# Kernel tuning notes

Hardware: AMD Instinct MI355X
Metric: run time of the kernel (lower is better)

Reference implementation:

```python
import jax, jax.numpy as jnp
import numpy as np

B, M, L, D, H, DFF, K, NL = 32, 512, 512, 128, 8, 256, 16, 2


def setup_inputs() -> dict:
    key = jax.random.key(0)
    ks = jax.random.split(key, 12)
    s = 0.02
    p = lambda i, shape: (jax.random.normal(ks[i], shape, jnp.float32) * s)
    return {
        "enc_out_vari": jax.random.normal(ks[0], (B, M, D), jnp.float32),
        "x_enc": jax.random.normal(ks[1], (B, L, M), jnp.float32),
        "conv1_W": p(2, (D, D)), "conv1_b": jnp.zeros((D,), jnp.float32),
        "conv2_W": p(3, (D, D)), "conv2_b": jnp.zeros((D,), jnp.float32),
        "Wq": p(4, (NL, D, D)), "Wk": p(5, (NL, D, D)),
        "Wv": p(6, (NL, D, D)), "Wo": p(7, (NL, D, D)),
        "ffn_W1": p(8, (NL, D, DFF)), "ffn_b1": jnp.zeros((NL, DFF), jnp.float32),
        "ffn_W2": p(9, (NL, DFF, D)), "ffn_b2": jnp.zeros((NL, D), jnp.float32),
        "ln1_g": jnp.ones((NL, D), jnp.float32), "ln1_b": jnp.zeros((NL, D), jnp.float32),
        "ln2_g": jnp.ones((NL, D), jnp.float32), "ln2_b": jnp.zeros((NL, D), jnp.float32),
    }


def _ln(x, g, b, eps=1e-5):
    mu = x.mean(-1, keepdims=True)
    var = ((x - mu) ** 2).mean(-1, keepdims=True)
    return (x - mu) * jax.lax.rsqrt(var + eps) * g + b


def _gcn_conv(x, src, dst, W, b, N):
    # PyG GCNConv: XW, add self loops, symmetric D^-1/2 (A+I) D^-1/2 aggregation, + bias
    h = x @ W
    loop = jnp.arange(N)
    s = jnp.concatenate([src, loop])
    d = jnp.concatenate([dst, loop])
    deg = jax.ops.segment_sum(jnp.ones_like(d, jnp.float32), d, num_segments=N)
    dinv = jnp.where(deg > 0, jax.lax.rsqrt(deg), 0.0)
    norm = dinv[s] * dinv[d]
    out = jax.ops.segment_sum(h[s] * norm[:, None], d, num_segments=N)
    return out + b


def _forward(enc_out_vari, x_enc, conv1_W, conv1_b, conv2_W, conv2_b,
             Wq, Wk, Wv, Wo, ffn_W1, ffn_b1, ffn_W2, ffn_b2,
             ln1_g, ln1_b, ln2_g, ln2_b):
    # --- dynamic graph from Pearson correlation (faithful: ascending argsort, idx 1..k) ---
    x = x_enc.transpose(0, 2, 1)                      # [B, M, L]
    c = x - x.mean(-1, keepdims=True)
    cov = jnp.einsum('bml,bnl->bmn', c, c) / (L - 1)  # [B, M, M]
    std = jnp.sqrt(jnp.diagonal(cov, axis1=-2, axis2=-1))
    std = jnp.where(std == 0, 1.0, std)
    corr = cov / (std[:, :, None] * std[:, None, :])
    neighbors = jnp.argsort(corr, axis=-1)[:, :, 1:K + 1]  # [B, M, K]
    row = jnp.tile(jnp.arange(M), K)                  # arange(M).repeat(k) in torch
    col = neighbors.reshape(B, M * K)
    offs = (jnp.arange(B) * M)[:, None]               # batch the graphs into one
    src = (row[None, :] + offs).reshape(-1)
    dst = (col + offs).reshape(-1)
    N = B * M
    # --- 2-layer GCN over flattened node set ---
    x_raw = enc_out_vari.reshape(N, D)
    h1 = jax.nn.relu(_gcn_conv(x_raw, src, dst, conv1_W, conv1_b, N))
    h2 = jax.nn.relu(_gcn_conv(h1, src, dst, conv2_W, conv2_b, N))
    xg = h2.reshape(B, M, D)
    # --- cross-attention transformer encoder: query stream = enc_out_vari, kv = GCN output ---
    h = enc_out_vari
    hd = D // H
    scale = 1.0 / jnp.sqrt(jnp.float32(hd))
    for l in range(NL):
        q = (h @ Wq[l]).reshape(B, M, H, hd)
        k_ = (xg @ Wk[l]).reshape(B, M, H, hd)
        v = (xg @ Wv[l]).reshape(B, M, H, hd)
        att = jax.nn.softmax(jnp.einsum('bqhd,bkhd->bhqk', q, k_) * scale, axis=-1)
        o = jnp.einsum('bhqk,bkhd->bqhd', att, v).reshape(B, M, D) @ Wo[l]
        h = _ln(h + o, ln1_g[l], ln1_b[l])
        f = jax.nn.relu(h @ ffn_W1[l] + ffn_b1[l]) @ ffn_W2[l] + ffn_b2[l]
        h = _ln(h + f, ln2_g[l], ln2_b[l])
    return h


def reference(enc_out_vari, x_enc, conv1_W, conv1_b, conv2_W, conv2_b,
              Wq, Wk, Wv, Wo, ffn_W1, ffn_b1, ffn_W2, ffn_b2,
              ln1_g, ln1_b, ln2_g, ln2_b):
    return _forward(enc_out_vari, x_enc, conv1_W, conv1_b, conv2_W, conv2_b,
                    Wq, Wk, Wv, Wo, ffn_W1, ffn_b1, ffn_W2, ffn_b2,
                    ln1_g, ln1_b, ln2_g, ln2_b)
```

## Files before the change

### kernel.cpp

```cpp
#include <hip/hip_runtime.h>
#include <float.h>

#define BB 32
#define MMv 512
#define LLv 512
#define DDv 128
#define HHv 8
#define DFFv 256
#define KNB 16
#define NLAY 2
#define NNODE (BB*MMv)
#define TOTE  (NNODE*KNB)
#define WTOT  294912

typedef unsigned short ushort_t;
typedef unsigned int u32;
typedef __attribute__((ext_vector_type(8))) short bf16x8;
typedef __attribute__((ext_vector_type(4))) float f32x4;

__device__ __forceinline__ float bf2f(ushort_t u){
  union { u32 i; float f; } x; x.i = ((u32)u) << 16; return x.f;
}
__device__ __forceinline__ ushort_t f2bf(float f){
  union { u32 i; float f; } x; x.f = f;
  u32 r = x.i + 0x7FFFu + ((x.i >> 16) & 1u);
  return (ushort_t)(r >> 16);
}
__device__ __forceinline__ float ldx(const void* p, size_t i, int f32){
  return f32 ? ((const float*)p)[i] : bf2f(((const ushort_t*)p)[i]);
}
__device__ __forceinline__ float wsum(float v){
  #pragma unroll
  for(int s=32;s;s>>=1) v += __shfl_xor(v,s);
  return v;
}

__global__ __launch_bounds__(256) void diag_fill_k(float* out, int n, float val){
  for(int i = blockIdx.x*256 + threadIdx.x; i < n; i += gridDim.x*256) out[i] = val;
}

struct P18 { const ushort_t* p[18]; int n[18]; };
__global__ __launch_bounds__(256) void ddet_k(P18 a, int* DF){
  int i = blockIdx.x;
  const ushort_t* q = a.p[i];
  int P = min(a.n[i], 4096);
  int t = threadIdx.x;
  int r1 = 0, evenNZ = 0, oddNZ = 0;
  for(int j=t; j<P; j+=256){
    ushort_t v = q[j];
    if(((v >> 7) & 0xFF) >= 0xC0) r1 = 1;
    if(v){ if(j & 1) oddNZ = 1; else evenNZ = 1; }
  }
  __shared__ int sh[3];
  if(t==0){ sh[0]=0; sh[1]=0; sh[2]=0; }
  __syncthreads();
  if(r1) atomicOr(&sh[0],1);
  if(evenNZ) atomicOr(&sh[1],1);
  if(oddNZ) atomicOr(&sh[2],1);
  __syncthreads();
  if(t==0) DF[i] = sh[0] | ((sh[1]==0) & (sh[2]!=0));
}

__global__ __launch_bounds__(256) void prep_k(const void* c1W, const void* c2W,
    const void* Wq, const void* Wk, const void* Wv, const void* Wo,
    const void* W1, const void* W2, ushort_t* Wth, ushort_t* Wtl, const int* DF){
  __shared__ ushort_t th[32][33];
  __shared__ ushort_t tl[32][33];
  int job = blockIdx.z;
  const void* src; int dfi; size_t soff, doff; int K, N;
  switch(job){
    case 0:  src=c1W; dfi=2;  soff=0; K=128; N=128; doff=0; break;
    case 1:  src=c2W; dfi=4;  soff=0; K=128; N=128; doff=16384; break;
    case 2: case 3:
      src=Wq; dfi=6; soff=(size_t)(job-2)*16384; K=128; N=128;
      doff=32768 + (size_t)(job-2)*49152; break;
    case 4: case 5:
      src=Wk; dfi=7; soff=(size_t)(job-4)*16384; K=128; N=128;
      doff=32768 + (size_t)(job-4)*49152 + 16384; break;
    case 6: case 7:
      src=Wv; dfi=8; soff=(size_t)(job-6)*16384; K=128; N=128;
      doff=32768 + (size_t)(job-6)*49152 + 32768; break;
    case 8: case 9:
      src=Wo; dfi=9; soff=(size_t)(job-8)*16384; K=128; N=128;
      doff=131072 + (size_t)(job-8)*16384; break;
    case 10: case 11:
      src=W1; dfi=10; soff=(size_t)(job-10)*32768; K=128; N=256;
      doff=163840 + (size_t)(job-10)*32768; break;
    default:
      src=W2; dfi=12; soff=(size_t)(job-12)*32768; K=256; N=128;
      doff=229376 + (size_t)(job-12)*32768; break;
  }
  int n0 = blockIdx.x*32, k0 = blockIdx.y*32;
  if(n0 >= N || k0 >= K) return;
  int f32 = DF[dfi];
  int tx = threadIdx.x, ty = threadIdx.y;
  #pragma unroll
  for(int i=0;i<4;i++){
    int k = k0+ty+8*i, n = n0+tx;
    float x = ldx(src, soff + (size_t)k*N + n, f32);
    ushort_t hi = f2bf(x);
    ushort_t lo = f2bf(x - bf2f(hi));
    th[ty+8*i][tx] = hi; tl[ty+8*i][tx] = lo;
  }
  __syncthreads();
  #pragma unroll
  for(int i=0;i<4;i++){
    int n = n0+ty+8*i, k = k0+tx;
    size_t d = doff + (size_t)n*K + k;
    Wth[d] = th[tx][ty+8*i];
    Wtl[d] = tl[tx][ty+8*i];
  }
}

__global__ __launch_bounds__(256) void split_k(const void* xe, ushort_t* Xhi,
                                               ushort_t* Xlo, const int* DF){
  __shared__ ushort_t th[32][33];
  __shared__ ushort_t tl[32][33];
  int f32 = DF[1];
  int b = blockIdx.z;
  int m0 = blockIdx.x*32, l0 = blockIdx.y*32;
  int tx = threadIdx.x, ty = threadIdx.y;
  #pragma unroll
  for(int i=0;i<4;i++){
    int l = l0+ty+8*i, m = m0+tx;
    float x = ldx(xe, (size_t)b*LLv*MMv + (size_t)l*MMv + m, f32);
    ushort_t hi = f2bf(x);
    ushort_t lo = f2bf(x - bf2f(hi));
    th[ty+8*i][tx] = hi; tl[ty+8*i][tx] = lo;
  }
  __syncthreads();
  #pragma unroll
  for(int i=0;i<4;i++){
    size_t d = (size_t)b*MMv*LLv + (size_t)(m0+ty+8*i)*LLv + l0+tx;
    Xhi[d] = th[tx][ty+8*i];
    Xlo[d] = tl[tx][ty+8*i];
  }
}

__global__ __launch_bounds__(256) void stats2_k(const ushort_t* Xhi, const ushort_t* Xlo,
                                                double* S64, double* R64){
  int row = blockIdx.x*4 + (threadIdx.x >> 6);
  int lane = threadIdx.x & 63;
  const ushort_t* Hr = Xhi + (size_t)row*LLv + lane*8;
  const ushort_t* Lr = Xlo + (size_t)row*LLv + lane*8;
  float s = 0.f, ss = 0.f;
  #pragma unroll
  for(int j=0;j<8;j++){
    float x = bf2f(Hr[j]) + bf2f(Lr[j]);
    s += x; ss = fmaf(x, x, ss);
  }
  s = wsum(s); ss = wsum(ss);
  if(lane == 0){
    S64[row] = (double)s;
    float cov = (ss - s*s*(1.0f/LLv)) * (1.0f/(LLv-1));
    float sd = (cov > 0.f) ? sqrtf(cov) : 0.f;
    R64[row] = (sd > 0.f) ? (double)(1.0f/sd) : 1.0;
  }
}

__global__ __launch_bounds__(1024, 8) void corrsel_k(const ushort_t* Xhi, const ushort_t* Xlo,
                                                     const double* S64, const double* R64,
                                                     int* nbr, const int* DF){
  __shared__ __attribute__((aligned(16))) char smem[66560];
  ushort_t* Ah = (ushort_t*)smem;
  ushort_t* Al = Ah + 32*520;
  float*    Cs = (float*)smem;
  int f32 = DF[1];
  int lin = blockIdx.y*16 + blockIdx.x;
  int xcd = lin & 7, slot = lin >> 3;
  int b = xcd + 8*(slot >> 4);
  int strip = slot & 15;
  int m0 = strip*32;
  int t = threadIdx.x;
  int wave = t >> 6, lane = t & 63;
  int quad = lane >> 4, l16 = lane & 15;
  const ushort_t* Hb = Xhi + (size_t)b*MMv*LLv;
  const ushort_t* Lb = Xlo + (size_t)b*MMv*LLv;
  for(int idx=t; idx<2048; idx+=1024){
    int mm = idx >> 6, c8 = (idx & 63)*8;
    *(bf16x8*)&Ah[mm*520 + c8] = *(const bf16x8*)&Hb[(size_t)(m0+mm)*LLv + c8];
    *(bf16x8*)&Al[mm*520 + c8] = *(const bf16x8*)&Lb[(size_t)(m0+mm)*LLv + c8];
  }
  __syncthreads();
  const double* Sb = S64 + b*MMv;
  const double* Rb = R64 + b*MMv;
  int nbase = wave*32;
  float corr[16];
  int nnv[2];
  #pragma unroll
  for(int cs=0; cs<2; cs++){
    int nn = nbase + cs*16 + l16;
    nnv[cs] = nn;
    size_t brow = (size_t)nn*LLv + quad*8;
    f32x4 acc0 = {0.f,0.f,0.f,0.f};
    f32x4 acc1 = {0.f,0.f,0.f,0.f};
    if(f32){
      #pragma unroll
      for(int kk=0; kk<16; kk++){
        int ko = kk*32 + quad*8;
        bf16x8 bh = *(const bf16x8*)&Hb[brow + kk*32];
        bf16x8 bl = *(const bf16x8*)&Lb[brow + kk*32];
        bf16x8 ah0 = *(const bf16x8*)&Ah[l16*520 + ko];
        bf16x8 al0 = *(const bf16x8*)&Al[l16*520 + ko];
        bf16x8 ah1 = *(const bf16x8*)&Ah[(16+l16)*520 + ko];
        bf16x8 al1 = *(const bf16x8*)&Al[(16+l16)*520 + ko];
        acc0 = __builtin_amdgcn_mfma_f32_16x16x32_bf16(ah0, bh, acc0, 0, 0, 0);
        acc0 = __builtin_amdgcn_mfma_f32_16x16x32_bf16(ah0, bl, acc0, 0, 0, 0);
        acc0 = __builtin_amdgcn_mfma_f32_16x16x32_bf16(al0, bh, acc0, 0, 0, 0);
        acc1 = __builtin_amdgcn_mfma_f32_16x16x32_bf16(ah1, bh, acc1, 0, 0, 0);
        acc1 = __builtin_amdgcn_mfma_f32_16x16x32_bf16(ah1, bl, acc1, 0, 0, 0);
        acc1 = __builtin_amdgcn_mfma_f32_16x16x32_bf16(al1, bh, acc1, 0, 0, 0);
      }
    } else {
      #pragma unroll
      for(int g=0; g<4; g++){
        bf16x8 bh[4];
        #pragma unroll
        for(int j=0;j<4;j++) bh[j] = *(const bf16x8*)&Hb[brow + g*128 + j*32];
        #pragma unroll
        for(int j=0;j<4;j++){
          int ko = g*128 + j*32 + quad*8;
          bf16x8 ah0 = *(const bf16x8*)&Ah[l16*520 + ko];
          bf16x8 ah1 = *(const bf16x8*)&Ah[(16+l16)*520 + ko];
          acc0 = __builtin_amdgcn_mfma_f32_16x16x32_bf16(ah0, bh[j], acc0, 0, 0, 0);
          acc1 = __builtin_amdgcn_mfma_f32_16x16x32_bf16(ah1, bh[j], acc1, 0, 0, 0);
        }
      }
    }
    float sn = (float)(Sb[nn]*(1.0/LLv));
    float rn = (float)Rb[nn];
    #pragma unroll
    for(int r=0;r<4;r++){
      int ml0 = quad*4 + r;
      float cov0 = (acc0[r] - (float)Sb[m0+ml0]*sn) * (1.0f/(LLv-1));
      corr[cs*8 + r] = cov0 * (float)Rb[m0+ml0] * rn;
      int ml1 = 16 + ml0;
      float cov1 = (acc1[r] - (float)Sb[m0+ml1]*sn) * (1.0f/(LLv-1));
      corr[cs*8 + 4 + r] = cov1 * (float)Rb[m0+ml1] * rn;
    }
  }
  __syncthreads();
  #pragma unroll
  for(int cs=0; cs<2; cs++){
    #pragma unroll
    for(int r=0;r<4;r++){
      int ml0 = quad*4 + r;
      Cs[ml0*516 + nnv[cs]] = corr[cs*8 + r];
      Cs[(16+ml0)*516 + nnv[cs]] = corr[cs*8 + 4 + r];
    }
  }
  __syncthreads();
  for(int rr=0; rr<2; rr++){
    int r = wave*2 + rr;
    float vals[8];
    #pragma unroll
    for(int j=0;j<8;j++) vals[j] = Cs[r*516 + lane + 64*j];
    for(int it=0; it<=KNB; it++){
      float bvv = FLT_MAX; int bi = 0x7fffffff;
      #pragma unroll
      for(int j=0;j<8;j++){
        int n = lane + 64*j;
        if(vals[j] < bvv){ bvv = vals[j]; bi = n; }
      }
      #pragma unroll
      for(int s=32; s; s>>=1){
        float v2 = __shfl_xor(bvv, s);
        int   i2 = __shfl_xor(bi,  s);
        if(v2 < bvv || (v2 == bvv && i2 < bi)){ bvv = v2; bi = i2; }
      }
      int gbi = bi;
      int bic = min(max(gbi, 0), MMv-1);
      if(it > 0 && lane == 0) nbr[(size_t)(b*MMv + m0 + r)*KNB + it-1] = bic;
      if((gbi & 63) == lane && gbi < MMv){
        int jj = gbi >> 6;
        #pragma unroll
        for(int j=0;j<8;j++) if(j == jj) vals[j] = FLT_MAX;
      }
    }
  }
}

__global__ __launch_bounds__(256) void zero_k(int* p){
  p[blockIdx.x*256 + threadIdx.x] = 0;
}

__global__ __launch_bounds__(256) void hist_k(const int* nbr, int* cnt){
  int tid = blockIdx.x*256 + threadIdx.x;
  int b = tid >> 13;
  int col = min(max(nbr[tid], 0), MMv-1);
  atomicAdd(&cnt[b*MMv + col], 1);
}

__global__ __launch_bounds__(256) void scan_k(const int* cnt, int* off,
                                              int* cursor, float* dinv){
  __shared__ int part[256];
  int t = threadIdx.x;
  int base = t*64, s = 0;
  for(int i=0;i<64;i++) s += cnt[base+i];
  part[t] = s; __syncthreads();
  for(int st=1; st<256; st<<=1){
    int v = (t >= st) ? part[t-st] : 0;
    __syncthreads();
    part[t] += v; __syncthreads();
  }
  int run = (t > 0) ? part[t-1] : 0;
  for(int i=0;i<64;i++){
    int idx = base+i;
    off[idx] = run; cursor[idx] = run;
    run += cnt[idx];
    dinv[idx] = 1.0f/sqrtf((float)(cnt[idx]+1));
  }
  if(t == 255) off[NNODE] = run;
}

__global__ __launch_bounds__(256) void fill_k(const int* nbr, int* cursor, int* esrc){
  int tid = blockIdx.x*256 + threadIdx.x;
  int b = tid >> 13;
  int rem = tid & 8191;
  int col = min(max(nbr[tid], 0), MMv-1);
  int dst = b*MMv + col;
  int srcl = rem & 511;
  int pos = atomicAdd(&cursor[dst], 1);
  pos = min(max(pos, 0), TOTE-1);
  esrc[pos] = b*MMv + srcl;
}

__global__ __launch_bounds__(256) void gemm_k(const float* A,
                                              const ushort_t* Wth, const ushort_t* Wtl,
                                              size_t woffT, int wdi,
                                              const void* bias, int boff, int bdi,
                                              float* C, int Kd, int Dout, int relu,
                                              const int* DF){
  __shared__ __attribute__((aligned(16))) ushort_t Ah[64*72];
  __shared__ __attribute__((aligned(16))) ushort_t Al[64*72];
  __shared__ __attribute__((aligned(16))) ushort_t Wh[32*72];
  __shared__ __attribute__((aligned(16))) ushort_t Wl[32*72];
  int wf32 = DF[wdi];
  int bf32 = DF[bdi];
  int m0 = blockIdx.y*64, n0 = blockIdx.x*32;
  int t = threadIdx.x;
  int wave = t >> 6, lane = t & 63;
  int quad = lane >> 4, l16 = lane & 15;
  f32x4 acc[2];
  #pragma unroll
  for(int nt=0;nt<2;nt++) acc[nt] = (f32x4){0.f,0.f,0.f,0.f};
  for(int kc=0; kc<Kd; kc+=64){
    for(int s=t; s<1024; s+=256){
      int row = s >> 4, c4 = (s & 15)*4;
      float4 av = *(const float4*)&A[(size_t)(m0+row)*Kd + kc + c4];
      ushort_t h0=f2bf(av.x), h1=f2bf(av.y), h2=f2bf(av.z), h3=f2bf(av.w);
      ushort_t g0=f2bf(av.x-bf2f(h0)), g1=f2bf(av.y-bf2f(h1));
      ushort_t g2=f2bf(av.z-bf2f(h2)), g3=f2bf(av.w-bf2f(h3));
      *(ushort4*)&Ah[row*72 + c4] = make_ushort4(h0,h1,h2,h3);
      *(ushort4*)&Al[row*72 + c4] = make_ushort4(g0,g1,g2,g3);
    }
    for(int s=t; s<256; s+=256){
      int row = s >> 3, c8 = (s & 7)*8;
      size_t g = woffT + (size_t)(n0+row)*Kd + kc + c8;
      *(bf16x8*)&Wh[row*72 + c8] = *(const bf16x8*)&Wth[g];
      if(wf32) *(bf16x8*)&Wl[row*72 + c8] = *(const bf16x8*)&Wtl[g];
    }
    __syncthreads();
    #pragma unroll
    for(int kk=0; kk<64; kk+=32){
      int ko = kk + quad*8;
      bf16x8 ah = *(const bf16x8*)&Ah[(wave*16+l16)*72 + ko];
      bf16x8 al = *(const bf16x8*)&Al[(wave*16+l16)*72 + ko];
      #pragma unroll
      for(int nt=0; nt<2; nt++){
        bf16x8 wh = *(const bf16x8*)&Wh[(nt*16+l16)*72 + ko];
        acc[nt] = __builtin_amdgcn_mfma_f32_16x16x32_bf16(ah, wh, acc[nt], 0, 0, 0);
        acc[nt] = __builtin_amdgcn_mfma_f32_16x16x32_bf16(al, wh, acc[nt], 0, 0, 0);
        if(wf32){
          bf16x8 wl = *(const bf16x8*)&Wl[(nt*16+l16)*72 + ko];
          acc[nt] = __builtin_amdgcn_mfma_f32_16x16x32_bf16(ah, wl, acc[nt], 0, 0, 0);
        }
      }
    }
    __syncthreads();
  }
  #pragma unroll
  for(int nt=0; nt<2; nt++){
    int n = n0 + nt*16 + l16;
    float bv = bias ? ldx(bias, boff + n, bf32) : 0.f;
    #pragma unroll
    for(int r=0; r<2*2; r++){
      float v = acc[nt][r] + bv;
      if(relu) v = fmaxf(v, 0.f);
      C[(size_t)(m0 + wave*16 + quad*4 + r)*Dout + n] = v;
    }
  }
}

__global__ __launch_bounds__(256) void qkv_k(const float* hF, const float* xg,
                                             const ushort_t* Wth, const ushort_t* Wtl,
                                             size_t qoff, float* t0, float* kv,
                                             const int* DF){
  __shared__ __attribute__((aligned(16))) ushort_t Ah[64*72];
  __shared__ __attribute__((aligned(16))) ushort_t Al[64*72];
  __shared__ __attribute__((aligned(16))) ushort_t Wh[32*72];
  __shared__ __attribute__((aligned(16))) ushort_t Wl[32*72];
  int m0 = blockIdx.y*64, n0 = blockIdx.x*32;
  int wdi = (n0 < 128) ? 6 : ((n0 < 256) ? 7 : 8);
  int wf32 = DF[wdi];
  const float* A = (n0 < 128) ? hF : xg;
  int t = threadIdx.x;
  int wave = t >> 6, lane = t & 63;
  int quad = lane >> 4, l16 = lane & 15;
  f32x4 acc[2];
  #pragma unroll
  for(int nt=0;nt<2;nt++) acc[nt] = (f32x4){0.f,0.f,0.f,0.f};
  for(int kc=0; kc<DDv; kc+=64){
    for(int s=t; s<1024; s+=256){
      int row = s >> 4, c4 = (s & 15)*4;
      float4 av = *(const float4*)&A[(size_t)(m0+row)*DDv + kc + c4];
      ushort_t h0=f2bf(av.x), h1=f2bf(av.y), h2=f2bf(av.z), h3=f2bf(av.w);
      ushort_t g0=f2bf(av.x-bf2f(h0)), g1=f2bf(av.y-bf2f(h1));
      ushort_t g2=f2bf(av.z-bf2f(h2)), g3=f2bf(av.w-bf2f(h3));
      *(ushort4*)&Ah[row*72 + c4] = make_ushort4(h0,h1,h2,h3);
      *(ushort4*)&Al[row*72 + c4] = make_ushort4(g0,g1,g2,g3);
    }
    for(int s=t; s<256; s+=256){
      int row = s >> 3, c8 = (s & 7)*8;
      size_t g = qoff + (size_t)(n0+row)*DDv + kc + c8;
      *(bf16x8*)&Wh[row*72 + c8] = *(const bf16x8*)&Wth[g];
      if(wf32) *(bf16x8*)&Wl[row*72 + c8] = *(const bf16x8*)&Wtl[g];
    }
    __syncthreads();
    #pragma unroll
    for(int kk=0; kk<64; kk+=32){
      int ko = kk + quad*8;
      bf16x8 ah = *(const bf16x8*)&Ah[(wave*16+l16)*72 + ko];
      bf16x8 al = *(const bf16x8*)&Al[(wave*16+l16)*72 + ko];
      #pragma unroll
      for(int nt=0; nt<2; nt++){
        bf16x8 wh = *(const bf16x8*)&Wh[(nt*16+l16)*72 + ko];
        acc[nt] = __builtin_amdgcn_mfma_f32_16x16x32_bf16(ah, wh, acc[nt], 0, 0, 0);
        acc[nt] = __builtin_amdgcn_mfma_f32_16x16x32_bf16(al, wh, acc[nt], 0, 0, 0);
        if(wf32){
          bf16x8 wl = *(const bf16x8*)&Wl[(nt*16+l16)*72 + ko];
          acc[nt] = __builtin_amdgcn_mfma_f32_16x16x32_bf16(ah, wl, acc[nt], 0, 0, 0);
        }
      }
    }
    __syncthreads();
  }
  float* C = (n0 < 128) ? t0 : kv;
  int ldC = (n0 < 128) ? 128 : 256;
  int nb  = (n0 < 128) ? n0 : (n0 - 128);
  #pragma unroll
  for(int nt=0; nt<2; nt++){
    int n = nb + nt*16 + l16;
    #pragma unroll
    for(int r=0; r<4; r++){
      C[(size_t)(m0 + wave*16 + quad*4 + r)*ldC + n] = acc[nt][r];
    }
  }
}

__global__ __launch_bounds__(256) void agg_k(const float* xw, const int* off,
                                             const int* esrc, const float* dinv,
                                             const void* bias, int bdi, float* out,
                                             const int* DF){
  int f32 = DF[bdi];
  int node = blockIdx.x*4 + (threadIdx.x >> 6);
  int lane = threadIdx.x & 63;
  float dn = dinv[node];
  float2 xv = ((const float2*)(xw + (size_t)node*DDv))[lane];
  float a0 = dn*dn*xv.x;
  float a1 = dn*dn*xv.y;
  int e0 = min(max(off[node], 0), TOTE);
  int e1 = min(max(off[node+1], e0), TOTE);
  int e = e0;
  for(; e + 4 <= e1; e += 4){
    int s0 = min(max(esrc[e+0], 0), NNODE-1);
    int s1 = min(max(esrc[e+1], 0), NNODE-1);
    int s2 = min(max(esrc[e+2], 0), NNODE-1);
    int s3 = min(max(esrc[e+3], 0), NNODE-1);
    float2 v0 = ((const float2*)(xw + (size_t)s0*DDv))[lane];
    float2 v1 = ((const float2*)(xw + (size_t)s1*DDv))[lane];
    float2 v2 = ((const float2*)(xw + (size_t)s2*DDv))[lane];
    float2 v3 = ((const float2*)(xw + (size_t)s3*DDv))[lane];
    float w0 = dinv[s0]*dn, w1 = dinv[s1]*dn, w2 = dinv[s2]*dn, w3 = dinv[s3]*dn;
    a0 = fmaf(w0, v0.x, a0); a1 = fmaf(w0, v0.y, a1);
    a0 = fmaf(w1, v1.x, a0); a1 = fmaf(w1, v1.y, a1);
    a0 = fmaf(w2, v2.x, a0); a1 = fmaf(w2, v2.y, a1);
    a0 = fmaf(w3, v3.x, a0); a1 = fmaf(w3, v3.y, a1);
  }
  for(; e < e1; e++){
    int s = min(max(esrc[e], 0), NNODE-1);
    float w = dinv[s]*dn;
    float2 sv = ((const float2*)(xw + (size_t)s*DDv))[lane];
    a0 = fmaf(w, sv.x, a0);
    a1 = fmaf(w, sv.y, a1);
  }
  a0 += ldx(bias, 2*lane, f32); a1 += ldx(bias, 2*lane+1, f32);
  ((float2*)(out + (size_t)node*DDv))[lane] = make_float2(fmaxf(a0,0.f), fmaxf(a1,0.f));
}

__global__ __launch_bounds__(1024) void attn_k(const float* qg, const float* kv,
                                               float* og){
  __shared__ float Ks[512*16];
  __shared__ float Vs[512*16];
  int bh = blockIdx.x;
  int b = bh >> 3, hh = bh & 7;
  size_t baseq = (size_t)b*MMv*DDv + (size_t)hh*16;
  size_t basekv = (size_t)b*MMv*256 + (size_t)hh*16;
  int t = threadIdx.x;
  for(int idx=t; idx<2048; idx+=1024){
    int kk = idx >> 2, i4 = (idx & 3)*4;
    ((float4*)Ks)[idx] = *(const float4*)&kv[basekv + (size_t)kk*256 + i4];
    ((float4*)Vs)[idx] = *(const float4*)&kv[basekv + (size_t)kk*256 + 128 + i4];
  }
  __syncthreads();
  int r = t & 511, g = t >> 9;
  float qr[16];
  #pragma unroll
  for(int i4=0;i4<4;i4++){
    float4 qv = *(const float4*)&qg[baseq + (size_t)r*DDv + i4*4];
    qr[i4*4+0]=qv.x; qr[i4*4+1]=qv.y; qr[i4*4+2]=qv.z; qr[i4*4+3]=qv.w;
  }
  float m = -FLT_MAX, l = 0.f;
  float acc[16] = {};
  int k0 = g*256;
  for(int kk=k0; kk<k0+256; kk++){
    const float* kp = &Ks[kk*16];
    float s = 0.f;
    #pragma unroll
    for(int i=0;i<16;i++) s = fmaf(qr[i], kp[i], s);
    s *= 0.25f;
    if(s > m){
      float c = __expf(m - s);
      l *= c;
      #pragma unroll
      for(int i=0;i<16;i++) acc[i] *= c;
      m = s;
    }
    float p = __expf(s - m);
    l += p;
    const float* vp = &Vs[kk*16];
    #pragma unroll
    for(int i=0;i<16;i++) acc[i] = fmaf(p, vp[i], acc[i]);
  }
  __syncthreads();
  if(g == 1){
    #pragma unroll
    for(int i=0;i<16;i++) Ks[r*16 + i] = acc[i];
    Vs[r] = m; Vs[512 + r] = l;
  }
  __syncthreads();
  if(g == 0){
    float m1 = Vs[r], l1 = Vs[512 + r];
    float M = fmaxf(m, m1);
    float c0 = __expf(m - M), c1 = __expf(m1 - M);
    float inv = 1.0f/(l*c0 + l1*c1);
    #pragma unroll
    for(int i=0;i<16;i++)
      og[baseq + (size_t)r*DDv + i] = (acc[i]*c0 + Ks[r*16 + i]*c1)*inv;
  }
}

__global__ __launch_bounds__(256) void ln_k(const float* h, const float* delta,
                                            const void* g, int gdi, const void* bb, int bdi, int po,
                                            float* dst, const int* DF){
  int gf32 = DF[gdi], bf32 = DF[bdi];
  int row = blockIdx.x*4 + (threadIdx.x >> 6);
  int lane = threadIdx.x & 63;
  const float2* hr = (const float2*)(h + (size_t)row*DDv);
  const float2* dr = (const float2*)(delta + (size_t)row*DDv);
  float2 hv = hr[lane], dv = dr[lane];
  float x0 = hv.x + dv.x, x1 = hv.y + dv.y;
  float mu = wsum(x0 + x1) * (1.0f/DDv);
  float d0 = x0 - mu, d1 = x1 - mu;
  float var = wsum(d0*d0 + d1*d1) * (1.0f/DDv);
  float rs = 1.0f/sqrtf(var + 1e-5f);
  int c0 = lane*2;
  float y0 = d0*rs*ldx(g, po+c0,   gf32) + ldx(bb, po+c0,   bf32);
  float y1 = d1*rs*ldx(g, po+c0+1, gf32) + ldx(bb, po+c0+1, bf32);
  ((float2*)(dst + (size_t)row*DDv))[lane] = make_float2(y0, y1);
}

__global__ __launch_bounds__(256) void cvt_k(const void* in, float* out, const int* DF){
  int f32 = DF[0];
  int tid = blockIdx.x*256 + threadIdx.x;
  out[tid] = ldx(in, tid, f32);
}

extern "C" void kernel_launch(void* const* d_in, const int* in_sizes, int n_in,
                              void* d_out, int out_size, void* d_ws, size_t ws_size,
                              hipStream_t stream) {
  if(n_in != 18){
    diag_fill_k<<<256, 256, 0, stream>>>((float*)d_out, out_size, 1000.0f);
    return;
  }
  const int expect[18] = {
    BB*MMv*DDv, BB*LLv*MMv, DDv*DDv, DDv, DDv*DDv, DDv,
    NLAY*DDv*DDv, NLAY*DDv*DDv, NLAY*DDv*DDv, NLAY*DDv*DDv,
    NLAY*DDv*DFFv, NLAY*DFFv, NLAY*DFFv*DDv, NLAY*DDv,
    NLAY*DDv, NLAY*DDv, NLAY*DDv, NLAY*DDv
  };
  for(int i=0;i<18;i++){
    if(in_sizes[i] != expect[i]){
      diag_fill_k<<<256, 256, 0, stream>>>((float*)d_out, out_size, 2000.0f + 10.0f*i);
      return;
    }
  }

  const void* enc  = d_in[0];
  const void* xe   = d_in[1];
  const void* c1W  = d_in[2];
  const void* c1b  = d_in[3];
  const void* c2W  = d_in[4];
  const void* c2b  = d_in[5];
  const void* Wq   = d_in[6];
  const void* Wk   = d_in[7];
  const void* Wv   = d_in[8];
  const void* Wo   = d_in[9];
  const void* W1   = d_in[10];
  const void* b1   = d_in[11];
  const void* W2   = d_in[12];
  const void* b2   = d_in[13];
  const void* ln1g = d_in[14];
  const void* ln1b = d_in[15];
  const void* ln2g = d_in[16];
  const void* ln2b = d_in[17];

  char* ws = (char*)d_ws;
  size_t o = 0;
  auto alloc = [&](size_t bytes){ size_t r = o; o = (o + bytes + 255) & ~(size_t)255; return r; };
  double* S64  = (double*)(ws + alloc((size_t)NNODE*8));
  double* R64  = (double*)(ws + alloc((size_t)NNODE*8));
  float* dinv  = (float*)(ws + alloc((size_t)NNODE*4));
  int*   cnt   = (int*)  (ws + alloc((size_t)NNODE*4));
  int*   cursor= (int*)  (ws + alloc((size_t)NNODE*4));
  int*   off   = (int*)  (ws + alloc((size_t)(NNODE+1)*4));
  int*   nbr   = (int*)  (ws + alloc((size_t)TOTE*4));
  int*   esrc  = (int*)  (ws + alloc((size_t)TOTE*4));
  int*   DF    = (int*)  (ws + alloc(256));
  ushort_t* Wth = (ushort_t*)(ws + alloc((size_t)WTOT*2));
  ushort_t* Wtl = (ushort_t*)(ws + alloc((size_t)WTOT*2));
  const size_t ACTF = (size_t)NNODE*DDv*4;
  float* hF = (float*)(ws + alloc(ACTF));
  float* xg = (float*)(ws + alloc(ACTF));
  float* t0 = (float*)(ws + alloc(ACTF));
  float* t1 = (float*)(ws + alloc(ACTF));
  float* t2 = (float*)(ws + alloc(ACTF));
  float* t3 = (float*)(ws + alloc(ACTF));
  float* kv = t1;
  float* fb = t1;
  ushort_t* Xhi = (ushort_t*)hF;
  ushort_t* Xlo = Xhi + (size_t)BB*MMv*LLv;
  if(ws_size < o){
    diag_fill_k<<<256, 256, 0, stream>>>((float*)d_out, out_size, 3000.0f);
    return;
  }

  P18 pack;
  for(int i=0;i<18;i++){ pack.p[i] = (const ushort_t*)d_in[i]; pack.n[i] = in_sizes[i]; }
  ddet_k<<<18, 256, 0, stream>>>(pack, DF);
  prep_k<<<dim3(8,8,14), dim3(32,8), 0, stream>>>(c1W, c2W, Wq, Wk, Wv, Wo, W1, W2,
                                                  Wth, Wtl, DF);

  split_k<<<dim3(16,16,BB), dim3(32,8), 0, stream>>>(xe, Xhi, Xlo, DF);
  stats2_k<<<NNODE/4, 256, 0, stream>>>(Xhi, Xlo, S64, R64);
  corrsel_k<<<dim3(16, BB), 1024, 0, stream>>>(Xhi, Xlo, S64, R64, nbr, DF);
  zero_k<<<NNODE/256, 256, 0, stream>>>(cnt);
  hist_k<<<TOTE/256, 256, 0, stream>>>(nbr, cnt);
  scan_k<<<1, 256, 0, stream>>>(cnt, off, cursor, dinv);
  fill_k<<<TOTE/256, 256, 0, stream>>>(nbr, cursor, esrc);

  cvt_k<<<NNODE*DDv/256, 256, 0, stream>>>(enc, hF, DF);
  gemm_k<<<dim3(4,256), 256, 0, stream>>>(hF, Wth, Wtl, 0, 2, nullptr, 0, 3, t0, DDv, DDv, 0, DF);
  agg_k<<<NNODE/4, 256, 0, stream>>>(t0, off, esrc, dinv, c1b, 3, t1, DF);
  gemm_k<<<dim3(4,256), 256, 0, stream>>>(t1, Wth, Wtl, 16384, 4, nullptr, 0, 5, t0, DDv, DDv, 0, DF);
  agg_k<<<NNODE/4, 256, 0, stream>>>(t0, off, esrc, dinv, c2b, 5, xg, DF);

  for(int l=0; l<NLAY; l++){
    qkv_k<<<dim3(12,256), 256, 0, stream>>>(hF, xg, Wth, Wtl,
                                            32768 + (size_t)l*49152, t0, kv, DF);
    attn_k<<<BB*HHv, 1024, 0, stream>>>(t0, kv, t3);
    gemm_k<<<dim3(4,256), 256, 0, stream>>>(t3, Wth, Wtl, 131072 + (size_t)l*16384, 9, nullptr, 0, 9, t0, DDv, DDv, 0, DF);
    ln_k<<<NNODE/4, 256, 0, stream>>>(hF, t0, ln1g, 14, ln1b, 15, l*DDv, hF, DF);
    gemm_k<<<dim3(8,256), 256, 0, stream>>>(hF, Wth, Wtl, 163840 + (size_t)l*32768, 10, b1, l*DFFv, 11, fb, DDv, DFFv, 1, DF);
    gemm_k<<<dim3(4,256), 256, 0, stream>>>(fb, Wth, Wtl, 229376 + (size_t)l*32768, 12, b2, l*DDv, 13, t0, DFFv, DDv, 0, DF);
    float* dst = (l == NLAY-1) ? (float*)d_out : hF;
    ln_k<<<NNODE/4, 256, 0, stream>>>(hF, t0, ln2g, 16, ln2b, 17, l*DDv, dst, DF);
  }
}
```

Baseline: 712.3 us.

## Halve corrsel row strip to 16 rows and double grid blocks

Each corrsel block now handles a 16-row strip instead of 32, so the grid doubles and each wave computes one 16x16 MFMA tile row per column chunk and selects neighbors for one row. Shared memory per block is halved, which can raise occupancy and spread work across more CUs. In exchange, each global load of the neighbor-column operand is reused for half as many rows, increasing global/L2 traffic and the number of Sb/Rb reads.

```diff
diff --git a/kernel.cpp b/kernel.cpp
--- a/kernel.cpp
+++ b/kernel.cpp
@@ -161,23 +161,23 @@
 __global__ __launch_bounds__(1024, 8) void corrsel_k(const ushort_t* Xhi, const ushort_t* Xlo,
                                                      const double* S64, const double* R64,
                                                      int* nbr, const int* DF){
-  __shared__ __attribute__((aligned(16))) char smem[66560];
+  __shared__ __attribute__((aligned(16))) char smem[33280];
   ushort_t* Ah = (ushort_t*)smem;
-  ushort_t* Al = Ah + 32*520;
+  ushort_t* Al = Ah + 16*520;
   float*    Cs = (float*)smem;
   int f32 = DF[1];
-  int lin = blockIdx.y*16 + blockIdx.x;
+  int lin = blockIdx.y*32 + blockIdx.x;
   int xcd = lin & 7, slot = lin >> 3;
-  int b = xcd + 8*(slot >> 4);
-  int strip = slot & 15;
-  int m0 = strip*32;
+  int b = xcd + 8*(slot >> 5);
+  int strip = slot & 31;
+  int m0 = strip*16;
   int t = threadIdx.x;
   int wave = t >> 6, lane = t & 63;
   int quad = lane >> 4, l16 = lane & 15;
   const ushort_t* Hb = Xhi + (size_t)b*MMv*LLv;
   const ushort_t* Lb = Xlo + (size_t)b*MMv*LLv;
-  for(int idx=t; idx<2048; idx+=1024){
-    int mm = idx >> 6, c8 = (idx & 63)*8;
+  {
+    int mm = t >> 6, c8 = (t & 63)*8;
     *(bf16x8*)&Ah[mm*520 + c8] = *(const bf16x8*)&Hb[(size_t)(m0+mm)*LLv + c8];
     *(bf16x8*)&Al[mm*520 + c8] = *(const bf16x8*)&Lb[(size_t)(m0+mm)*LLv + c8];
   }
@@ -185,31 +185,23 @@
   const double* Sb = S64 + b*MMv;
   const double* Rb = R64 + b*MMv;
   int nbase = wave*32;
-  float corr[16];
-  int nnv[2];
+  float corr[8];
   #pragma unroll
   for(int cs=0; cs<2; cs++){
     int nn = nbase + cs*16 + l16;
-    nnv[cs] = nn;
     size_t brow = (size_t)nn*LLv + quad*8;
-    f32x4 acc0 = {0.f,0.f,0.f,0.f};
-    f32x4 acc1 = {0.f,0.f,0.f,0.f};
+    f32x4 acc = {0.f,0.f,0.f,0.f};
     if(f32){
       #pragma unroll
       for(int kk=0; kk<16; kk++){
         int ko = kk*32 + quad*8;
         bf16x8 bh = *(const bf16x8*)&Hb[brow + kk*32];
         bf16x8 bl = *(const bf16x8*)&Lb[brow + kk*32];
-        bf16x8 ah0 = *(const bf16x8*)&Ah[l16*520 + ko];
-        bf16x8 al0 = *(const bf16x8*)&Al[l16*520 + ko];
-        bf16x8 ah1 = *(const bf16x8*)&Ah[(16+l16)*520 + ko];
-        bf16x8 al1 = *(const bf16x8*)&Al[(16+l16)*520 + ko];
-        acc0 = __builtin_amdgcn_mfma_f32_16x16x32_bf16(ah0, bh, acc0, 0, 0, 0);
-        acc0 = __builtin_amdgcn_mfma_f32_16x16x32_bf16(ah0, bl, acc0, 0, 0, 0);
-        acc0 = __builtin_amdgcn_mfma_f32_16x16x32_bf16(al0, bh, acc0, 0, 0, 0);
-        acc1 = __builtin_amdgcn_mfma_f32_16x16x32_bf16(ah1, bh, acc1, 0, 0, 0);
-        acc1 = __builtin_amdgcn_mfma_f32_16x16x32_bf16(ah1, bl, acc1, 0, 0, 0);
-        acc1 = __builtin_amdgcn_mfma_f32_16x16x32_bf16(al1, bh, acc1, 0, 0, 0);
+        bf16x8 ah = *(const bf16x8*)&Ah[l16*520 + ko];
+        bf16x8 al = *(const bf16x8*)&Al[l16*520 + ko];
+        acc = __builtin_amdgcn_mfma_f32_16x16x32_bf16(ah, bh, acc, 0, 0, 0);
+        acc = __builtin_amdgcn_mfma_f32_16x16x32_bf16(ah, bl, acc, 0, 0, 0);
+        acc = __builtin_amdgcn_mfma_f32_16x16x32_bf16(al, bh, acc, 0, 0, 0);
       }
     } else {
       #pragma unroll
@@ -220,10 +212,8 @@
         #pragma unroll
         for(int j=0;j<4;j++){
           int ko = g*128 + j*32 + quad*8;
-          bf16x8 ah0 = *(const bf16x8*)&Ah[l16*520 + ko];
-          bf16x8 ah1 = *(const bf16x8*)&Ah[(16+l16)*520 + ko];
-          acc0 = __builtin_amdgcn_mfma_f32_16x16x32_bf16(ah0, bh[j], acc0, 0, 0, 0);
-          acc1 = __builtin_amdgcn_mfma_f32_16x16x32_bf16(ah1, bh[j], acc1, 0, 0, 0);
+          bf16x8 ah = *(const bf16x8*)&Ah[l16*520 + ko];
+          acc = __builtin_amdgcn_mfma_f32_16x16x32_bf16(ah, bh[j], acc, 0, 0, 0);
         }
       }
     }
@@ -231,27 +221,23 @@
     float rn = (float)Rb[nn];
     #pragma unroll
     for(int r=0;r<4;r++){
-      int ml0 = quad*4 + r;
-      float cov0 = (acc0[r] - (float)Sb[m0+ml0]*sn) * (1.0f/(LLv-1));
-      corr[cs*8 + r] = cov0 * (float)Rb[m0+ml0] * rn;
-      int ml1 = 16 + ml0;
-      float cov1 = (acc1[r] - (float)Sb[m0+ml1]*sn) * (1.0f/(LLv-1));
-      corr[cs*8 + 4 + r] = cov1 * (float)Rb[m0+ml1] * rn;
+      int ml = quad*4 + r;
+      float cov = (acc[r] - (float)Sb[m0+ml]*sn) * (1.0f/(LLv-1));
+      corr[cs*4 + r] = cov * (float)Rb[m0+ml] * rn;
     }
   }
   __syncthreads();
   #pragma unroll
   for(int cs=0; cs<2; cs++){
+    int nn = nbase + cs*16 + l16;
     #pragma unroll
     for(int r=0;r<4;r++){
-      int ml0 = quad*4 + r;
-      Cs[ml0*516 + nnv[cs]] = corr[cs*8 + r];
-      Cs[(16+ml0)*516 + nnv[cs]] = corr[cs*8 + 4 + r];
-    }
-  }
-  __syncthreads();
-  for(int rr=0; rr<2; rr++){
-    int r = wave*2 + rr;
+      Cs[(quad*4 + r)*516 + nn] = corr[cs*4 + r];
+    }
+  }
+  __syncthreads();
+  {
+    int r = wave;
     float vals[8];
     #pragma unroll
     for(int j=0;j<8;j++) vals[j] = Cs[r*516 + lane + 64*j];
@@ -663,7 +649,7 @@
 
   split_k<<<dim3(16,16,BB), dim3(32,8), 0, stream>>>(xe, Xhi, Xlo, DF);
   stats2_k<<<NNODE/4, 256, 0, stream>>>(Xhi, Xlo, S64, R64);
-  corrsel_k<<<dim3(16, BB), 1024, 0, stream>>>(Xhi, Xlo, S64, R64, nbr, DF);
+  corrsel_k<<<dim3(32, BB), 1024, 0, stream>>>(Xhi, Xlo, S64, R64, nbr, DF);
   zero_k<<<NNODE/256, 256, 0, stream>>>(cnt);
   hist_k<<<TOTE/256, 256, 0, stream>>>(nbr, cnt);
   scan_k<<<1, 256, 0, stream>>>(cnt, off, cursor, dinv);
```

Measured after the change: 739.8 us. 3.9% more time.
